# Optimization experiments

Hardware: AMD Instinct MI355X
Metric: run time of the kernel (lower is better)

## Reference

```python
import jax, jax.numpy as jnp
import numpy as np

D = 128          # embed_features
N = 4096         # cells per batch
M = 8192         # genes / regions
FB1, FB2, FR, FA = 100, 100, 256, 512


def setup_inputs() -> dict:
    key = jax.random.key(0)
    ks = jax.random.split(key, 16)
    s = 0.05  # weight scale to keep activations in a sane range
    return {
        "u1": jax.random.normal(ks[0], (N, FB1), jnp.float32),
        "u2": jax.random.normal(ks[1], (N, FB2), jnp.float32),
        "v1": jax.random.normal(ks[2], (M, FR), jnp.float32),
        "v2": jax.random.normal(ks[3], (M, FA), jnp.float32),
        # linear layers stored as [in, out] so y = x @ W
        "Wb1": jax.random.normal(ks[4], (FB1, D), jnp.float32) * s,
        "Wb2": jax.random.normal(ks[5], (FB2, D), jnp.float32) * s,
        "Wrna1": jax.random.normal(ks[6], (FR, 2 * D), jnp.float32) * s,
        "Wrna2": jax.random.normal(ks[7], (2 * D, D), jnp.float32) * s,
        "gene_act": jax.random.normal(ks[8], (FA, FR), jnp.float32) * s,
        "w_prod1": jax.random.normal(ks[9], (D,), jnp.float32),
        "w_add1": jax.random.normal(ks[10], (2 * D,), jnp.float32),
        "w_prod2": jax.random.normal(ks[11], (D,), jnp.float32),
        "w_add2": jax.random.normal(ks[12], (2 * D,), jnp.float32),
        "bias_1": jax.random.normal(ks[13], (), jnp.float32),
        "bias_2": jax.random.normal(ks[14], (), jnp.float32),
    }


def _pair_scores(eu, ev, w_prod, w_add, bias):
    # Algebraically identical to the original all-pairs form:
    #   (eu[:,None,:] * ev[None,:,:]) @ w_prod  ==  (eu * w_prod) @ ev.T
    #   cat(eu, ev) @ w_add  ==  eu @ w_add[:D]  +  ev @ w_add[D:]
    prod = (eu * w_prod) @ ev.T                     # [N, M]
    add = (eu @ w_add[:D])[:, None] + (ev @ w_add[D:])[None, :]
    return prod + add + bias                        # [N, M]


def reference(u1, u2, v1, v2, Wb1, Wb2, Wrna1, Wrna2, gene_act,
              w_prod1, w_add1, w_prod2, w_add2, bias_1, bias_2):
    # mode='linear' activations -> identity
    embed_u1 = u1 @ Wb1                                          # [N, D]
    embed_v1 = jax.nn.relu(v1 @ Wrna1) @ Wrna2                   # [M, D]
    out1 = jax.nn.relu(_pair_scores(embed_u1, embed_v1, w_prod1, w_add1, bias_1))

    embed_u2 = u2 @ Wb2                                          # [N, D]
    embed_v2 = jax.nn.relu((v2 @ gene_act) @ Wrna1) @ Wrna2      # [M, D]
    out2 = jax.nn.sigmoid(_pair_scores(embed_u2, embed_v2, w_prod2, w_add2, bias_2))

    return out1, out2, embed_u1, embed_v1, embed_u2, embed_v2
```

## Files before the change

kernel.cpp:

```cpp
#include <hip/hip_runtime.h>
#include <math.h>

#define N_CELLS 4096
#define M_GENES 8192

typedef __attribute__((ext_vector_type(8))) short short8;
typedef __attribute__((ext_vector_type(4))) float f32x4;

__device__ __align__(16) float g_a[24576];

__device__ __align__(16) short g_bu1[N_CELLS * 128];
__device__ __align__(16) short g_bv1[M_GENES * 128];
__device__ __align__(16) short g_bu2[N_CELLS * 128];
__device__ __align__(16) short g_bv2[M_GENES * 128];

__device__ __align__(16) short g_gaT[256 * 512];
__device__ __align__(16) short g_W1T[256 * 256];
__device__ __align__(16) short g_W2T[128 * 256];
__device__ __align__(16) short g_ub1[N_CELLS * 128];
__device__ __align__(16) short g_ub2[N_CELLS * 128];
__device__ __align__(16) short g_WbT1[128 * 128];
__device__ __align__(16) short g_WbT2[128 * 128];


__device__ __forceinline__ short* bf_sel(int s) {
    switch (s) {
        case 0:  return g_bu1;
        case 1:  return g_bv1;
        case 2:  return g_bu2;
        default: return g_bv2;
    }
}

__device__ __forceinline__ const short* wt_sel(int s) {
    switch (s) {
        case 0:  return g_gaT;
        case 1:  return g_W1T;
        default: return g_W2T;
    }
}

__device__ __forceinline__ short f2bf(float f) {
    unsigned u = __builtin_bit_cast(unsigned, f);
    u += 0x7FFFu + ((u >> 16) & 1u);
    return (short)(u >> 16);
}

__device__ __forceinline__ void cvt8(const float* __restrict__ in, short* __restrict__ out) {
    const float4 x0 = *reinterpret_cast<const float4*>(in);
    const float4 x1 = *reinterpret_cast<const float4*>(in + 4);
    short8 o;
    o[0] = f2bf(x0.x); o[1] = f2bf(x0.y); o[2] = f2bf(x0.z); o[3] = f2bf(x0.w);
    o[4] = f2bf(x1.x); o[5] = f2bf(x1.y); o[6] = f2bf(x1.z); o[7] = f2bf(x1.w);
    *reinterpret_cast<short8*>(out) = o;
}

__device__ __forceinline__ void transpose8(const float* __restrict__ in, short* __restrict__ out,
                                           int c, int K, int Nc) {
    const int o0 = c * 8;
    const int ncol = o0 / K;
    const int k0 = o0 % K;
    short8 o;
#pragma unroll
    for (int j = 0; j < 8; ++j) o[j] = f2bf(in[(size_t)(k0 + j) * Nc + ncol]);
    *reinterpret_cast<short8*>(out + o0) = o;
}

__device__ __forceinline__ void stage_A_f32(char* cA, const float* Af, int row0, int k0, int K, int t)
{
    const float* gAf = Af + (size_t)row0 * K + k0;
#pragma unroll
    for (int c = 0; c < 4; ++c) {
        const int idx = c * 256 + t;
        const int row = idx >> 4, sub = idx & 15;
        const int dst = row * 256 + ((sub * 16) ^ ((row & 7) << 4));
        cvt8(gAf + (size_t)row * K + sub * 8, (short*)(cA + dst));
    }
}

__device__ __forceinline__ void stage_B128(char* cB, const short* BT, int col0, int k0, int K, int t)
{
    const char* gB = (const char*)(BT + (size_t)col0 * K + k0);
#pragma unroll
    for (int c = 0; c < 8; ++c) {
        const int idx = c * 256 + t;
        const int row = idx >> 4, sub = idx & 15;
        const int dst = row * 256 + ((sub * 16) ^ ((row & 7) << 4));
        *(short8*)(cB + dst) = *(const short8*)(gB + (size_t)row * (2 * K) + sub * 16);
    }
}

__device__ __forceinline__ void stage_B64(char* cB, const short* BT, int col0, int k0, int K, int t)
{
    const char* gB = (const char*)(BT + (size_t)col0 * K + k0);
#pragma unroll
    for (int c = 0; c < 4; ++c) {
        const int idx = c * 256 + t;
        const int row = idx >> 4, sub = idx & 15;
        const int dst = row * 256 + ((sub * 16) ^ ((row & 7) << 4));
        *(short8*)(cB + dst) = *(const short8*)(gB + (size_t)row * (2 * K) + sub * 16);
    }
}

__device__ __forceinline__ void mfma128(const char* cA, int strideA, int baseA,
                                        const char* cB, f32x4 (&acc)[2][4], int t)
{
    const int l = t & 63, w = t >> 6;
    const int wm = (w >> 1) * 32, wn = (w & 1) * 64;
    const int lr = l & 15, lkb = (l >> 4) * 16;
#pragma unroll
    for (int kk = 0; kk < 4; ++kk) {
        const int kb = kk * 64 + lkb;
        short8 a[2], b4[4];
#pragma unroll
        for (int i = 0; i < 2; ++i) {
            const int rA = wm + i * 16 + lr;
            a[i] = *(const short8*)(cA + rA * strideA + ((baseA + kb) ^ ((rA & 7) << 4)));
        }
#pragma unroll
        for (int jj = 0; jj < 4; ++jj) {
            const int rB = wn + jj * 16 + lr;
            b4[jj] = *(const short8*)(cB + rB * 256 + (kb ^ ((rB & 7) << 4)));
        }
#pragma unroll
        for (int i = 0; i < 2; ++i)
#pragma unroll
            for (int jj = 0; jj < 4; ++jj)
                acc[i][jj] = __builtin_amdgcn_mfma_f32_16x16x32_bf16(a[i], b4[jj], acc[i][jj], 0, 0, 0);
    }
}

__device__ __forceinline__ void mfma64(const char* cA, int strideA, int baseA,
                                       const char* cB, f32x4 (&acc)[4], int t)
{
    const int l = t & 63, w = t >> 6;
    const int wm = w * 16;
    const int lr = l & 15, lkb = (l >> 4) * 16;
#pragma unroll
    for (int kk = 0; kk < 4; ++kk) {
        const int kb = kk * 64 + lkb;
        const int rA = wm + lr;
        const short8 a = *(const short8*)(cA + rA * strideA + ((baseA + kb) ^ ((rA & 7) << 4)));
#pragma unroll
        for (int jj = 0; jj < 4; ++jj) {
            const int rB = jj * 16 + lr;
            const short8 b = *(const short8*)(cB + rB * 256 + (kb ^ ((rB & 7) << 4)));
            acc[jj] = __builtin_amdgcn_mfma_f32_16x16x32_bf16(a, b, acc[jj], 0, 0, 0);
        }
    }
}

__device__ __forceinline__ void acc_to_sH(char* sH, const f32x4 (&acc)[2][4], int ct, bool relu, int t)
{
    const int l = t & 63, w = t >> 6;
    const int wm = (w >> 1) * 32, wn = (w & 1) * 64;
    const int lr = l & 15, r4 = (l >> 4) * 4;
#pragma unroll
    for (int i = 0; i < 2; ++i)
#pragma unroll
        for (int r = 0; r < 4; ++r) {
            const int row = wm + i * 16 + r4 + r;
#pragma unroll
            for (int jj = 0; jj < 4; ++jj) {
                float x = acc[i][jj][r];
                if (relu) x = fmaxf(x, 0.f);
                const int col = ct * 128 + wn + jj * 16 + lr;
                *(short*)(sH + row * 512 + ((col * 2) ^ ((row & 7) << 4))) = f2bf(x);
            }
        }
}

__device__ __forceinline__ void acc2_to_sH(char* sH, const f32x4 (&a4)[4], int ct, bool relu, int t)
{
    const int l = t & 63, w = t >> 6;
    const int lr = l & 15, r4 = (l >> 4) * 4;
#pragma unroll
    for (int r = 0; r < 4; ++r) {
        const int row = w * 16 + r4 + r;
#pragma unroll
        for (int jj = 0; jj < 4; ++jj) {
            float x = a4[jj][r];
            if (relu) x = fmaxf(x, 0.f);
            const int col = ct * 64 + jj * 16 + lr;
            *(short*)(sH + row * 512 + ((col * 2) ^ ((row & 7) << 4))) = f2bf(x);
        }
    }
}

__device__ __forceinline__ void first_layer(const float* Vf, int row0, int KV, int bsel, bool relu,
                                            char* cA, char* cH, int t)
{
    const short* BT = wt_sel(bsel);
    f32x4 accA[2][4] = {}, accB[2][4] = {};
    for (int k0 = 0; k0 < KV; k0 += 128) {
        stage_A_f32(cA, Vf, row0, k0, KV, t);
        stage_B128(cH, BT, 0, k0, KV, t);
        __syncthreads();
        mfma128(cA, 256, 0, cH, accA, t);
        __syncthreads();
        stage_B128(cH, BT, 128, k0, KV, t);
        __syncthreads();
        mfma128(cA, 256, 0, cH, accB, t);
        __syncthreads();
    }
    acc_to_sH(cH, accA, 0, relu, t);
    acc_to_sH(cH, accB, 1, relu, t);
    __syncthreads();
}

__device__ __forceinline__ void mid_layer(char* cH, char* cB64, int t)
{
    const short* W1T = wt_sel(1);
    f32x4 h4[4][4];
#pragma unroll
    for (int ct = 0; ct < 4; ++ct)
#pragma unroll
        for (int jj = 0; jj < 4; ++jj) h4[ct][jj] = (f32x4){0.f, 0.f, 0.f, 0.f};
#pragma unroll
    for (int ct = 0; ct < 4; ++ct)
        for (int k0 = 0; k0 < 2; ++k0) {
            stage_B64(cB64, W1T, ct * 64, k0 * 128, 256, t);
            __syncthreads();
            mfma64(cH, 512, k0 * 256, cB64, h4[ct], t);
            __syncthreads();
        }
#pragma unroll
    for (int ct = 0; ct < 4; ++ct) acc2_to_sH(cH, h4[ct], ct, true, t);
    __syncthreads();
}

__device__ __forceinline__ void final_layer(char* cH, char* cB64, float* evout, short* bv,
                                            const float* w_add_hi, int a_ofs, int row0, int t)
{
    const short* W2T = wt_sel(2);
    const int l = t & 63, w = t >> 6, lr = l & 15, r4 = (l >> 4) * 4;
    float part[4] = {0.f, 0.f, 0.f, 0.f};
#pragma unroll
    for (int ct = 0; ct < 2; ++ct) {
        f32x4 a2[4] = {};
        for (int k0 = 0; k0 < 2; ++k0) {
            stage_B64(cB64, W2T, ct * 64, k0 * 128, 256, t);
            __syncthreads();
            mfma64(cH, 512, k0 * 256, cB64, a2, t);
            __syncthreads();
        }
#pragma unroll
        for (int r = 0; r < 4; ++r) {
            const int grow = row0 + w * 16 + r4 + r;
#pragma unroll
            for (int jj = 0; jj < 4; ++jj) {
                const float x = a2[jj][r];
                const int col = ct * 64 + jj * 16 + lr;
                evout[(size_t)grow * 128 + col] = x;
                bv[(size_t)grow * 128 + col] = f2bf(x);
                part[r] = fmaf(x, w_add_hi[col], part[r]);
            }
        }
    }
#pragma unroll
    for (int off = 1; off < 16; off <<= 1)
#pragma unroll
        for (int r = 0; r < 4; ++r) part[r] += __shfl_xor(part[r], off, 64);
    if (lr == 0) {
#pragma unroll
        for (int r = 0; r < 4; ++r) g_a[a_ofs + row0 + w * 16 + r4 + r] = part[r];
    }
}

__global__ __launch_bounds__(256) void prep_all2(const float* __restrict__ gene_act,
                                                 const float* __restrict__ W1,
                                                 const float* __restrict__ W2,
                                                 const float* __restrict__ u1,
                                                 const float* __restrict__ u2,
                                                 const float* __restrict__ Wb1,
                                                 const float* __restrict__ Wb2)
{
    const int b = blockIdx.x, t = threadIdx.x;
    if (b < 64)       transpose8(gene_act, g_gaT, b * 256 + t, 512, 256);
    else if (b < 96)  transpose8(W1, g_W1T, (b - 64) * 256 + t, 256, 256);
    else if (b < 112) transpose8(W2, g_W2T, (b - 96) * 256 + t, 256, 128);
    else if (b < 624) {
        const int which = (b >= 368);
        const int c = (b - (which ? 368 : 112)) * 256 + t;
        const float* u = which ? u2 : u1;
        short* ub = which ? g_ub2 : g_ub1;
        const int row = c >> 4, sub = c & 15;
        short8 o = {0, 0, 0, 0, 0, 0, 0, 0};
        if (sub < 12) {
            const float4 x0 = *(const float4*)(u + row * 100 + sub * 8);
            const float4 x1 = *(const float4*)(u + row * 100 + sub * 8 + 4);
            o[0] = f2bf(x0.x); o[1] = f2bf(x0.y); o[2] = f2bf(x0.z); o[3] = f2bf(x0.w);
            o[4] = f2bf(x1.x); o[5] = f2bf(x1.y); o[6] = f2bf(x1.z); o[7] = f2bf(x1.w);
        } else if (sub == 12) {
            const float4 x0 = *(const float4*)(u + row * 100 + 96);
            o[0] = f2bf(x0.x); o[1] = f2bf(x0.y); o[2] = f2bf(x0.z); o[3] = f2bf(x0.w);
        }
        *(short8*)(ub + (size_t)c * 8) = o;
    } else {
        const int which = (b >= 632);
        const int c = (b - (which ? 632 : 624)) * 256 + t;
        const float* Wb = which ? Wb2 : Wb1;
        short* wt = which ? g_WbT2 : g_WbT1;
        const int col = c >> 4, k0 = (c & 15) * 8;
        short8 o;
#pragma unroll
        for (int j = 0; j < 8; ++j)
            o[j] = (k0 + j < 100) ? f2bf(Wb[(size_t)(k0 + j) * 128 + col]) : (short)0;
        *(short8*)(wt + (size_t)c * 8) = o;
    }
}

__global__ __launch_bounds__(256) void fused_mid(const float* __restrict__ v1,
                                                 const float* __restrict__ v2,
                                                 const float* __restrict__ wp1,
                                                 const float* __restrict__ wa1,
                                                 const float* __restrict__ wp2,
                                                 const float* __restrict__ wa2,
                                                 float* __restrict__ eu1,
                                                 float* __restrict__ eu2,
                                                 float* __restrict__ ev1,
                                                 float* __restrict__ ev2)
{
    __shared__ __align__(16) short sMem[32768];
    char* cA   = (char*)sMem;
    char* cB64 = cA + 16384;
    char* cH   = cA + 32768;
    const int b = blockIdx.x, t = threadIdx.x;
    if (b < 128) {
        const int row0 = b * 64;
        first_layer(v2, row0, 512, 0, false, cA, cH, t);
        mid_layer(cH, cB64, t);
        final_layer(cH, cB64, ev2, bf_sel(3), wa2 + 128, 16384, row0, t);
    } else if (b < 256) {
        const int row0 = (b - 128) * 64;
        first_layer(v1, row0, 256, 1, true, cA, cH, t);
        final_layer(cH, cB64, ev1, bf_sel(1), wa1 + 128, 4096, row0, t);
    } else {
        const int eb = b - 256;
        const int which = eb >> 6;
        const int row0 = (eb & 63) * 64;
        const short* Au  = which ? g_ub2  : g_ub1;
        const short* WbT = which ? g_WbT2 : g_WbT1;
        const float* wp = which ? wp2 : wp1;
        const float* wa = which ? wa2 : wa1;
        float* eu = which ? eu2 : eu1;
        short* bu = bf_sel(which ? 2 : 0);
        const int a_ofs = which ? 12288 : 0;

        stage_B64(cA, Au, row0, 0, 128, t);
        stage_B128(cH, WbT, 0, 0, 128, t);
        __syncthreads();
        f32x4 acc[2][4] = {};
        mfma128(cA, 256, 0, cH, acc, t);
        __syncthreads();

        const int l = t & 63, w = t >> 6;
        const int wm = (w >> 1) * 32, wn = (w & 1) * 64;
        const int lr = l & 15, r4 = (l >> 4) * 4;
        float* sRow = (float*)cB64;
        float wvp[4], wva[4];
#pragma unroll
        for (int jj = 0; jj < 4; ++jj) {
            const int col = wn + jj * 16 + lr;
            wvp[jj] = wp[col];
            wva[jj] = wa[col];
        }
        float part[2][4] = {};
#pragma unroll
        for (int i = 0; i < 2; ++i)
#pragma unroll
            for (int r = 0; r < 4; ++r) {
                const int grow = row0 + wm + i * 16 + r4 + r;
#pragma unroll
                for (int jj = 0; jj < 4; ++jj) {
                    const float x = acc[i][jj][r];
                    const int col = wn + jj * 16 + lr;
                    eu[(size_t)grow * 128 + col] = x;
                    bu[(size_t)grow * 128 + col] = f2bf(x * wvp[jj]);
                    part[i][r] = fmaf(x, wva[jj], part[i][r]);
                }
            }
#pragma unroll
        for (int off = 1; off < 16; off <<= 1)
#pragma unroll
            for (int i = 0; i < 2; ++i)
#pragma unroll
                for (int r = 0; r < 4; ++r)
                    part[i][r] += __shfl_xor(part[i][r], off, 64);
        if (t < 64) sRow[t] = 0.f;
        __syncthreads();
        if (lr == 0) {
#pragma unroll
            for (int i = 0; i < 2; ++i)
#pragma unroll
                for (int r = 0; r < 4; ++r)
                    atomicAdd(&sRow[wm + i * 16 + r4 + r], part[i][r]);
        }
        __syncthreads();
        if (t < 64) g_a[a_ofs + row0 + t] = sRow[t];
    }
}

__global__ __launch_bounds__(256) void pair_both(const float* __restrict__ bias1,
                                                 const float* __restrict__ bias2,
                                                 float* __restrict__ out1,
                                                 float* __restrict__ out2)
{
    __shared__ __align__(16) short sA[128 * 128];
    __shared__ __align__(16) short sB[128 * 128];
    const int which = blockIdx.z;
    const int t = threadIdx.x;
    const int l = t & 63;
    const int row0 = blockIdx.y * 128;
    const int col0 = blockIdx.x * 128;

    {
        const short8* gA = reinterpret_cast<const short8*>(bf_sel(which ? 2 : 0)) + (size_t)row0 * 16;
        const short8* gB = reinterpret_cast<const short8*>(bf_sel(which ? 3 : 1)) + (size_t)col0 * 16;
        char* cA = (char*)sA;
        char* cB = (char*)sB;
#pragma unroll
        for (int c = 0; c < 8; ++c) {
            const int idx = c * 256 + t;
            const int row = idx >> 4, sub = idx & 15;
            const int dst = row * 256 + ((sub * 16) ^ ((row & 7) << 4));
            const short8 va = gA[idx];
            const short8 vb = gB[idx];
            *(short8*)(cA + dst) = va;
            *(short8*)(cB + dst) = vb;
        }
    }
    __syncthreads();

    const int w  = t >> 6;
    const int wm = (w >> 1) * 64;
    const int wn = (w & 1) * 64;
    const int lr = l & 15;
    const int lkb = (l >> 4) * 16;

    f32x4 acc[4][4] = {};
    const char* cA = (const char*)sA;
    const char* cB = (const char*)sB;
#pragma unroll
    for (int kk = 0; kk < 4; ++kk) {
        const int kb = kk * 64 + lkb;
        short8 a[4], bfr[4];
#pragma unroll
        for (int i = 0; i < 4; ++i) {
            const int rowA = wm + i * 16 + lr;
            a[i] = *(const short8*)(cA + rowA * 256 + (kb ^ ((rowA & 7) << 4)));
            const int rowB = wn + i * 16 + lr;
            bfr[i] = *(const short8*)(cB + rowB * 256 + (kb ^ ((rowB & 7) << 4)));
        }
#pragma unroll
        for (int i = 0; i < 4; ++i)
#pragma unroll
            for (int jj = 0; jj < 4; ++jj)
                acc[i][jj] = __builtin_amdgcn_mfma_f32_16x16x32_bf16(a[i], bfr[jj], acc[i][jj], 0, 0, 0);
    }

    const float bias = which ? *bias2 : *bias1;
    float* outp = which ? out2 : out1;
    const int ofsU = which ? 12288 : 0;
    const int ofsV = which ? 16384 : 4096;
    const int r4 = (l >> 4) * 4;
    float au[4][4];
#pragma unroll
    for (int i = 0; i < 4; ++i)
#pragma unroll
        for (int r = 0; r < 4; ++r)
            au[i][r] = g_a[ofsU + row0 + wm + i * 16 + r4 + r];
    float av[4];
#pragma unroll
    for (int jj = 0; jj < 4; ++jj)
        av[jj] = g_a[ofsV + col0 + wn + jj * 16 + lr];

#pragma unroll
    for (int i = 0; i < 4; ++i) {
#pragma unroll
        for (int r = 0; r < 4; ++r) {
            const int grow = row0 + wm + i * 16 + r4 + r;
            float* orow = outp + (size_t)grow * M_GENES + col0 + wn;
#pragma unroll
            for (int jj = 0; jj < 4; ++jj) {
                float x = acc[i][jj][r] + au[i][r] + av[jj] + bias;
                if (which == 0) x = fmaxf(x, 0.f);
                else            x = __builtin_amdgcn_rcpf(1.f + __expf(-x));
                orow[jj * 16 + lr] = x;
            }
        }
    }
}

extern "C" void kernel_launch(void* const* d_in, const int* in_sizes, int n_in,
                              void* d_out, int out_size, void* d_ws, size_t ws_size,
                              hipStream_t stream)
{
    const float* u1       = (const float*)d_in[0];
    const float* u2       = (const float*)d_in[1];
    const float* v1       = (const float*)d_in[2];
    const float* v2       = (const float*)d_in[3];
    const float* Wb1      = (const float*)d_in[4];
    const float* Wb2      = (const float*)d_in[5];
    const float* Wrna1    = (const float*)d_in[6];
    const float* Wrna2    = (const float*)d_in[7];
    const float* gene_act = (const float*)d_in[8];
    const float* w_prod1  = (const float*)d_in[9];
    const float* w_add1   = (const float*)d_in[10];
    const float* w_prod2  = (const float*)d_in[11];
    const float* w_add2   = (const float*)d_in[12];
    const float* bias1    = (const float*)d_in[13];
    const float* bias2    = (const float*)d_in[14];

    float* out  = (float*)d_out;
    float* out1 = out;
    float* out2 = out1 + (size_t)N_CELLS * M_GENES;
    float* eu1  = out2 + (size_t)N_CELLS * M_GENES;
    float* ev1  = eu1 + N_CELLS * 128;
    float* eu2  = ev1 + M_GENES * 128;
    float* ev2  = eu2 + N_CELLS * 128;

    prep_all2<<<640, 256, 0, stream>>>(gene_act, Wrna1, Wrna2, u1, u2, Wb1, Wb2);

    fused_mid<<<384, 256, 0, stream>>>(v1, v2, w_prod1, w_add1, w_prod2, w_add2,
                                       eu1, eu2, ev1, ev2);

    pair_both<<<dim3(64, 32, 2), 256, 0, stream>>>(bias1, bias2, out1, out2);
}
```

Measured before the change: 115.9 us.

## Overlap v2 embedding chain with pair1 tiles and use nontemporal output stores

Splits the middle stage so the cheap v1 and u embeddings run first. The expensive v2 three-layer chain then runs as extra blocks inside the same launch as the out1 pair tiles, and a final kernel computes the out2 tiles. The goal is to hide the long v2 chain behind the bandwidth-bound out1 writes instead of serializing it. It also switches output writes to nontemporal stores to reduce cache pollution. The cost is one more kernel launch, and the pair tiles now run in a kernel that reserves the larger shared-memory footprint.

```diff
diff --git a/kernel.cpp b/kernel.cpp
--- a/kernel.cpp
+++ b/kernel.cpp
@@ -264,6 +264,155 @@
     if (lr == 0) {
 #pragma unroll
         for (int r = 0; r < 4; ++r) g_a[a_ofs + row0 + w * 16 + r4 + r] = part[r];
+    }
+}
+
+__device__ __forceinline__ void embed_mfma(int eb, const float* wp1, const float* wa1,
+                                           const float* wp2, const float* wa2,
+                                           float* eu1, float* eu2,
+                                           char* cA, char* cB64, char* cH, int t)
+{
+    const int which = eb >> 6;
+    const int row0 = (eb & 63) * 64;
+    const short* Au  = which ? g_ub2  : g_ub1;
+    const short* WbT = which ? g_WbT2 : g_WbT1;
+    const float* wp = which ? wp2 : wp1;
+    const float* wa = which ? wa2 : wa1;
+    float* eu = which ? eu2 : eu1;
+    short* bu = bf_sel(which ? 2 : 0);
+    const int a_ofs = which ? 12288 : 0;
+
+    stage_B64(cA, Au, row0, 0, 128, t);
+    stage_B128(cH, WbT, 0, 0, 128, t);
+    __syncthreads();
+    f32x4 acc[2][4] = {};
+    mfma128(cA, 256, 0, cH, acc, t);
+    __syncthreads();
+
+    const int l = t & 63, w = t >> 6;
+    const int wm = (w >> 1) * 32, wn = (w & 1) * 64;
+    const int lr = l & 15, r4 = (l >> 4) * 4;
+    float* sRow = (float*)cB64;
+    float wvp[4], wva[4];
+#pragma unroll
+    for (int jj = 0; jj < 4; ++jj) {
+        const int col = wn + jj * 16 + lr;
+        wvp[jj] = wp[col];
+        wva[jj] = wa[col];
+    }
+    float part[2][4] = {};
+#pragma unroll
+    for (int i = 0; i < 2; ++i)
+#pragma unroll
+        for (int r = 0; r < 4; ++r) {
+            const int grow = row0 + wm + i * 16 + r4 + r;
+#pragma unroll
+            for (int jj = 0; jj < 4; ++jj) {
+                const float x = acc[i][jj][r];
+                const int col = wn + jj * 16 + lr;
+                eu[(size_t)grow * 128 + col] = x;
+                bu[(size_t)grow * 128 + col] = f2bf(x * wvp[jj]);
+                part[i][r] = fmaf(x, wva[jj], part[i][r]);
+            }
+        }
+#pragma unroll
+    for (int off = 1; off < 16; off <<= 1)
+#pragma unroll
+        for (int i = 0; i < 2; ++i)
+#pragma unroll
+            for (int r = 0; r < 4; ++r)
+                part[i][r] += __shfl_xor(part[i][r], off, 64);
+    if (t < 64) sRow[t] = 0.f;
+    __syncthreads();
+    if (lr == 0) {
+#pragma unroll
+        for (int i = 0; i < 2; ++i)
+#pragma unroll
+            for (int r = 0; r < 4; ++r)
+                atomicAdd(&sRow[wm + i * 16 + r4 + r], part[i][r]);
+    }
+    __syncthreads();
+    if (t < 64) g_a[a_ofs + row0 + t] = sRow[t];
+}
+
+__device__ __forceinline__ void pair_tile(int which, int bb, char* cA, char* cB,
+                                          const float* bias1, const float* bias2,
+                                          float* out1, float* out2, int t)
+{
+    const int l = t & 63;
+    const int col0 = (bb & 63) * 128;
+    const int row0 = (bb >> 6) * 128;
+    {
+        const short8* gA = reinterpret_cast<const short8*>(bf_sel(which ? 2 : 0)) + (size_t)row0 * 16;
+        const short8* gB = reinterpret_cast<const short8*>(bf_sel(which ? 3 : 1)) + (size_t)col0 * 16;
+#pragma unroll
+        for (int c = 0; c < 8; ++c) {
+            const int idx = c * 256 + t;
+            const int row = idx >> 4, sub = idx & 15;
+            const int dst = row * 256 + ((sub * 16) ^ ((row & 7) << 4));
+            const short8 va = gA[idx];
+            const short8 vb = gB[idx];
+            *(short8*)(cA + dst) = va;
+            *(short8*)(cB + dst) = vb;
+        }
+    }
+    __syncthreads();
+
+    const int w  = t >> 6;
+    const int wm = (w >> 1) * 64;
+    const int wn = (w & 1) * 64;
+    const int lr = l & 15;
+    const int lkb = (l >> 4) * 16;
+
+    f32x4 acc[4][4] = {};
+#pragma unroll
+    for (int kk = 0; kk < 4; ++kk) {
+        const int kb = kk * 64 + lkb;
+        short8 a[4], bfr[4];
+#pragma unroll
+        for (int i = 0; i < 4; ++i) {
+            const int rowA = wm + i * 16 + lr;
+            a[i] = *(const short8*)(cA + rowA * 256 + (kb ^ ((rowA & 7) << 4)));
+            const int rowB = wn + i * 16 + lr;
+            bfr[i] = *(const short8*)(cB + rowB * 256 + (kb ^ ((rowB & 7) << 4)));
+        }
+#pragma unroll
+        for (int i = 0; i < 4; ++i)
+#pragma unroll
+            for (int jj = 0; jj < 4; ++jj)
+                acc[i][jj] = __builtin_amdgcn_mfma_f32_16x16x32_bf16(a[i], bfr[jj], acc[i][jj], 0, 0, 0);
+    }
+
+    const float bias = which ? *bias2 : *bias1;
+    float* outp = which ? out2 : out1;
+    const int ofsU = which ? 12288 : 0;
+    const int ofsV = which ? 16384 : 4096;
+    const int r4 = (l >> 4) * 4;
+    float au[4][4];
+#pragma unroll
+    for (int i = 0; i < 4; ++i)
+#pragma unroll
+        for (int r = 0; r < 4; ++r)
+            au[i][r] = g_a[ofsU + row0 + wm + i * 16 + r4 + r];
+    float av[4];
+#pragma unroll
+    for (int jj = 0; jj < 4; ++jj)
+        av[jj] = g_a[ofsV + col0 + wn + jj * 16 + lr];
+
+#pragma unroll
+    for (int i = 0; i < 4; ++i) {
+#pragma unroll
+        for (int r = 0; r < 4; ++r) {
+            const int grow = row0 + wm + i * 16 + r4 + r;
+            float* orow = outp + (size_t)grow * M_GENES + col0 + wn;
+#pragma unroll
+            for (int jj = 0; jj < 4; ++jj) {
+                float x = acc[i][jj][r] + au[i][r] + av[jj] + bias;
+                if (which == 0) x = fmaxf(x, 0.f);
+                else            x = __builtin_amdgcn_rcpf(1.f + __expf(-x));
+                __builtin_nontemporal_store(x, orow + jj * 16 + lr);
+            }
+        }
     }
 }
 
@@ -310,16 +459,36 @@
     }
 }
 
-__global__ __launch_bounds__(256) void fused_mid(const float* __restrict__ v1,
-                                                 const float* __restrict__ v2,
-                                                 const float* __restrict__ wp1,
-                                                 const float* __restrict__ wa1,
-                                                 const float* __restrict__ wp2,
-                                                 const float* __restrict__ wa2,
-                                                 float* __restrict__ eu1,
-                                                 float* __restrict__ eu2,
-                                                 float* __restrict__ ev1,
-                                                 float* __restrict__ ev2)
+__global__ __launch_bounds__(256) void fused_s1(const float* __restrict__ v1,
+                                                const float* __restrict__ wp1,
+                                                const float* __restrict__ wa1,
+                                                const float* __restrict__ wp2,
+                                                const float* __restrict__ wa2,
+                                                float* __restrict__ eu1,
+                                                float* __restrict__ eu2,
+                                                float* __restrict__ ev1)
+{
+    __shared__ __align__(16) short sMem[32768];
+    char* cA   = (char*)sMem;
+    char* cB64 = cA + 16384;
+    char* cH   = cA + 32768;
+    const int b = blockIdx.x, t = threadIdx.x;
+    if (b < 128) {
+        const int row0 = b * 64;
+        first_layer(v1, row0, 256, 1, true, cA, cH, t);
+        final_layer(cH, cB64, ev1, bf_sel(1), wa1 + 128, 4096, row0, t);
+    } else {
+        embed_mfma(b - 128, wp1, wa1, wp2, wa2, eu1, eu2, cA, cB64, cH, t);
+    }
+}
+
+__global__ __launch_bounds__(256) void pair1_s2(const float* __restrict__ v2,
+                                                const float* __restrict__ wa2,
+                                                float* __restrict__ ev2,
+                                                const float* __restrict__ bias1,
+                                                const float* __restrict__ bias2,
+                                                float* __restrict__ out1,
+                                                float* __restrict__ out2)
 {
     __shared__ __align__(16) short sMem[32768];
     char* cA   = (char*)sMem;
@@ -331,165 +500,19 @@
         first_layer(v2, row0, 512, 0, false, cA, cH, t);
         mid_layer(cH, cB64, t);
         final_layer(cH, cB64, ev2, bf_sel(3), wa2 + 128, 16384, row0, t);
-    } else if (b < 256) {
-        const int row0 = (b - 128) * 64;
-        first_layer(v1, row0, 256, 1, true, cA, cH, t);
-        final_layer(cH, cB64, ev1, bf_sel(1), wa1 + 128, 4096, row0, t);
     } else {
-        const int eb = b - 256;
-        const int which = eb >> 6;
-        const int row0 = (eb & 63) * 64;
-        const short* Au  = which ? g_ub2  : g_ub1;
-        const short* WbT = which ? g_WbT2 : g_WbT1;
-        const float* wp = which ? wp2 : wp1;
-        const float* wa = which ? wa2 : wa1;
-        float* eu = which ? eu2 : eu1;
-        short* bu = bf_sel(which ? 2 : 0);
-        const int a_ofs = which ? 12288 : 0;
-
-        stage_B64(cA, Au, row0, 0, 128, t);
-        stage_B128(cH, WbT, 0, 0, 128, t);
-        __syncthreads();
-        f32x4 acc[2][4] = {};
-        mfma128(cA, 256, 0, cH, acc, t);
-        __syncthreads();
-
-        const int l = t & 63, w = t >> 6;
-        const int wm = (w >> 1) * 32, wn = (w & 1) * 64;
-        const int lr = l & 15, r4 = (l >> 4) * 4;
-        float* sRow = (float*)cB64;
-        float wvp[4], wva[4];
-#pragma unroll
-        for (int jj = 0; jj < 4; ++jj) {
-            const int col = wn + jj * 16 + lr;
-            wvp[jj] = wp[col];
-            wva[jj] = wa[col];
-        }
-        float part[2][4] = {};
-#pragma unroll
-        for (int i = 0; i < 2; ++i)
-#pragma unroll
-            for (int r = 0; r < 4; ++r) {
-                const int grow = row0 + wm + i * 16 + r4 + r;
-#pragma unroll
-                for (int jj = 0; jj < 4; ++jj) {
-                    const float x = acc[i][jj][r];
-                    const int col = wn + jj * 16 + lr;
-                    eu[(size_t)grow * 128 + col] = x;
-                    bu[(size_t)grow * 128 + col] = f2bf(x * wvp[jj]);
-                    part[i][r] = fmaf(x, wva[jj], part[i][r]);
-                }
-            }
-#pragma unroll
-        for (int off = 1; off < 16; off <<= 1)
-#pragma unroll
-            for (int i = 0; i < 2; ++i)
-#pragma unroll
-                for (int r = 0; r < 4; ++r)
-                    part[i][r] += __shfl_xor(part[i][r], off, 64);
-        if (t < 64) sRow[t] = 0.f;
-        __syncthreads();
-        if (lr == 0) {
-#pragma unroll
-            for (int i = 0; i < 2; ++i)
-#pragma unroll
-                for (int r = 0; r < 4; ++r)
-                    atomicAdd(&sRow[wm + i * 16 + r4 + r], part[i][r]);
-        }
-        __syncthreads();
-        if (t < 64) g_a[a_ofs + row0 + t] = sRow[t];
-    }
-}
-
-__global__ __launch_bounds__(256) void pair_both(const float* __restrict__ bias1,
-                                                 const float* __restrict__ bias2,
-                                                 float* __restrict__ out1,
-                                                 float* __restrict__ out2)
-{
-    __shared__ __align__(16) short sA[128 * 128];
-    __shared__ __align__(16) short sB[128 * 128];
-    const int which = blockIdx.z;
-    const int t = threadIdx.x;
-    const int l = t & 63;
-    const int row0 = blockIdx.y * 128;
-    const int col0 = blockIdx.x * 128;
-
-    {
-        const short8* gA = reinterpret_cast<const short8*>(bf_sel(which ? 2 : 0)) + (size_t)row0 * 16;
-        const short8* gB = reinterpret_cast<const short8*>(bf_sel(which ? 3 : 1)) + (size_t)col0 * 16;
-        char* cA = (char*)sA;
-        char* cB = (char*)sB;
-#pragma unroll
-        for (int c = 0; c < 8; ++c) {
-            const int idx = c * 256 + t;
-            const int row = idx >> 4, sub = idx & 15;
-            const int dst = row * 256 + ((sub * 16) ^ ((row & 7) << 4));
-            const short8 va = gA[idx];
-            const short8 vb = gB[idx];
-            *(short8*)(cA + dst) = va;
-            *(short8*)(cB + dst) = vb;
-        }
-    }
-    __syncthreads();
-
-    const int w  = t >> 6;
-    const int wm = (w >> 1) * 64;
-    const int wn = (w & 1) * 64;
-    const int lr = l & 15;
-    const int lkb = (l >> 4) * 16;
-
-    f32x4 acc[4][4] = {};
-    const char* cA = (const char*)sA;
-    const char* cB = (const char*)sB;
-#pragma unroll
-    for (int kk = 0; kk < 4; ++kk) {
-        const int kb = kk * 64 + lkb;
-        short8 a[4], bfr[4];
-#pragma unroll
-        for (int i = 0; i < 4; ++i) {
-            const int rowA = wm + i * 16 + lr;
-            a[i] = *(const short8*)(cA + rowA * 256 + (kb ^ ((rowA & 7) << 4)));
-            const int rowB = wn + i * 16 + lr;
-            bfr[i] = *(const short8*)(cB + rowB * 256 + (kb ^ ((rowB & 7) << 4)));
-        }
-#pragma unroll
-        for (int i = 0; i < 4; ++i)
-#pragma unroll
-            for (int jj = 0; jj < 4; ++jj)
-                acc[i][jj] = __builtin_amdgcn_mfma_f32_16x16x32_bf16(a[i], bfr[jj], acc[i][jj], 0, 0, 0);
-    }
-
-    const float bias = which ? *bias2 : *bias1;
-    float* outp = which ? out2 : out1;
-    const int ofsU = which ? 12288 : 0;
-    const int ofsV = which ? 16384 : 4096;
-    const int r4 = (l >> 4) * 4;
-    float au[4][4];
-#pragma unroll
-    for (int i = 0; i < 4; ++i)
-#pragma unroll
-        for (int r = 0; r < 4; ++r)
-            au[i][r] = g_a[ofsU + row0 + wm + i * 16 + r4 + r];
-    float av[4];
-#pragma unroll
-    for (int jj = 0; jj < 4; ++jj)
-        av[jj] = g_a[ofsV + col0 + wn + jj * 16 + lr];
-
-#pragma unroll
-    for (int i = 0; i < 4; ++i) {
-#pragma unroll
-        for (int r = 0; r < 4; ++r) {
-            const int grow = row0 + wm + i * 16 + r4 + r;
-            float* orow = outp + (size_t)grow * M_GENES + col0 + wn;
-#pragma unroll
-            for (int jj = 0; jj < 4; ++jj) {
-                float x = acc[i][jj][r] + au[i][r] + av[jj] + bias;
-                if (which == 0) x = fmaxf(x, 0.f);
-                else            x = __builtin_amdgcn_rcpf(1.f + __expf(-x));
-                orow[jj * 16 + lr] = x;
-            }
-        }
-    }
+        pair_tile(0, b - 128, cA, cA + 32768, bias1, bias2, out1, out2, t);
+    }
+}
+
+__global__ __launch_bounds__(256) void pair2_k(const float* __restrict__ bias1,
+                                               const float* __restrict__ bias2,
+                                               float* __restrict__ out1,
+                                               float* __restrict__ out2)
+{
+    __shared__ __align__(16) short sMem[32768];
+    pair_tile(1, blockIdx.x, (char*)sMem, (char*)sMem + 32768, bias1, bias2,
+              out1, out2, threadIdx.x);
 }
 
 extern "C" void kernel_launch(void* const* d_in, const int* in_sizes, int n_in,
@@ -522,8 +545,10 @@
 
     prep_all2<<<640, 256, 0, stream>>>(gene_act, Wrna1, Wrna2, u1, u2, Wb1, Wb2);
 
-    fused_mid<<<384, 256, 0, stream>>>(v1, v2, w_prod1, w_add1, w_prod2, w_add2,
-                                       eu1, eu2, ev1, ev2);
-
-    pair_both<<<dim3(64, 32, 2), 256, 0, stream>>>(bias1, bias2, out1, out2);
-}
+    fused_s1<<<256, 256, 0, stream>>>(v1, w_prod1, w_add1, w_prod2, w_add2,
+                                      eu1, eu2, ev1);
+
+    pair1_s2<<<2176, 256, 0, stream>>>(v2, w_add2, ev2, bias1, bias2, out1, out2);
+
+    pair2_k<<<2048, 256, 0, stream>>>(bias1, bias2, out1, out2);
+}
```

Result: faster. 107.6 us (-7.1%).
